# Optimization experiments

Hardware: AMD Instinct MI355X
Metric: run time of the kernel (lower is better)

Reference implementation:

```python
import jax, jax.numpy as jnp
import numpy as np

N_HEADS = 32
KV_HEADS = 8
HEAD_DIM = 128
N_REP = N_HEADS // KV_HEADS


def _rope(x, cos, sin):
    # x: [b, s, h, d]; cos/sin: [s, d//2]
    xr = x[..., 0::2]
    xi = x[..., 1::2]
    c = cos[None, :, None, :]
    s = sin[None, :, None, :]
    or_ = xr * c - xi * s
    oi_ = xr * s + xi * c
    return jnp.stack([or_, oi_], axis=-1).reshape(x.shape)


def setup_inputs() -> dict:
    key = jax.random.key(0)
    ks = jax.random.split(key, 9)
    b, s, dim = 32, 1, 4096
    scale = 1.0 / np.sqrt(dim)
    inp = {
        "x": jax.random.normal(ks[0], (b, s, dim), jnp.float32),
        "wq": jax.random.normal(ks[1], (4096, 4096), jnp.float32) * scale,
        "wk": jax.random.normal(ks[2], (1024, 4096), jnp.float32) * scale,
        "wv": jax.random.normal(ks[3], (1024, 4096), jnp.float32) * scale,
        "wo": jax.random.normal(ks[4], (4096, 4096), jnp.float32) * scale,
        "freqs_cos": jax.random.uniform(ks[5], (s, HEAD_DIM // 2), jnp.float32),
        "freqs_sin": jax.random.uniform(ks[6], (s, HEAD_DIM // 2), jnp.float32),
        "cache_k": jax.random.normal(ks[7], (32, 2048, KV_HEADS, HEAD_DIM), jnp.float32),
        "cache_v": jax.random.normal(ks[8], (32, 2048, KV_HEADS, HEAD_DIM), jnp.float32),
        "start_pos": 2047,
    }
    return inp


def reference(x, wq, wk, wv, wo, freqs_cos, freqs_sin, cache_k, cache_v, start_pos):
    b, s, dim = x.shape
    # projections (nn.Linear: y = x @ W^T)
    xq = (x @ wq.T).reshape(b, s, N_HEADS, HEAD_DIM)
    xk = (x @ wk.T).reshape(b, s, KV_HEADS, HEAD_DIM)
    xv = (x @ wv.T).reshape(b, s, KV_HEADS, HEAD_DIM)
    # inline RoPE on q and k
    xq = _rope(xq, freqs_cos, freqs_sin)
    xk = _rope(xk, freqs_cos, freqs_sin)
    # KV-cache write (start_pos is a static Python int)
    cache_k = cache_k.at[:b, start_pos:start_pos + s].set(xk)
    cache_v = cache_v.at[:b, start_pos:start_pos + s].set(xv)
    t = start_pos + s
    keys = cache_k[:b, :t]    # [b, t, kv, d]
    values = cache_v[:b, :t]  # [b, t, kv, d]
    # GQA: group queries per kv head instead of materializing repeat_kv copies
    q = xq.reshape(b, s, KV_HEADS, N_REP, HEAD_DIM)
    scores = jnp.einsum("bqhrd,bkhd->bhrqk", q, keys) / np.sqrt(HEAD_DIM)
    probs = jax.nn.softmax(scores.astype(jnp.float32), axis=-1).astype(xq.dtype)
    out = jnp.einsum("bhrqk,bkhd->bqhrd", probs, values)
    out = out.reshape(b, s, N_HEADS * HEAD_DIM)
    return out @ wo.T
```

## Files before the change

### kernel.cpp

```cpp
#include <hip/hip_runtime.h>
#include <hip/hip_bf16.h>
#include <math.h>

#define KSPLIT 16
#define KCHUNK 256
#define BJ 128
#define TSPLIT 4

__global__ __launch_bounds__(256) void gemv_part_kernel(
    const float* __restrict__ x,
    const float* __restrict__ w0,
    const float* __restrict__ w1,
    const float* __restrict__ w2,
    int jb1, int jb2,
    int off0, int off1, int off2,
    int ncols,
    float* __restrict__ part)
{
  __shared__ float xt[KCHUNK][32];
  int jb = blockIdx.x, ks = blockIdx.y;
  int k0 = ks * KCHUNK;
  const float* w; int colOff, jbase;
  if (jb < jb1)      { w = w0; colOff = off0; jbase = jb * BJ; }
  else if (jb < jb2) { w = w1; colOff = off1; jbase = (jb - jb1) * BJ; }
  else               { w = w2; colOff = off2; jbase = (jb - jb2) * BJ; }
  int tid = threadIdx.x;
  {
    int b = tid & 31, kg = tid >> 5;
    const float* xr = x + (size_t)b * 4096 + k0 + kg * 32;
    #pragma unroll
    for (int i = 0; i < 8; i++) {
      float4 v = *(const float4*)(xr + i * 4);
      int k = kg * 32 + i * 4;
      xt[k + 0][b] = v.x; xt[k + 1][b] = v.y;
      xt[k + 2][b] = v.z; xt[k + 3][b] = v.w;
    }
  }
  __syncthreads();
  int bg = tid & 7, jg = tid >> 3;
  const float* wb = w + (size_t)(jbase + jg * 4) * 4096 + k0;
  float acc[4][4] = {};
  #pragma unroll 4
  for (int k4 = 0; k4 < KCHUNK / 4; k4++) {
    float wr[4][4], xv[4][4];
    #pragma unroll
    for (int jj = 0; jj < 4; jj++) {
      float4 t = *(const float4*)(wb + (size_t)jj * 4096 + k4 * 4);
      wr[jj][0] = t.x; wr[jj][1] = t.y; wr[jj][2] = t.z; wr[jj][3] = t.w;
    }
    #pragma unroll
    for (int c = 0; c < 4; c++) {
      float4 t = *(const float4*)(&xt[k4 * 4 + c][bg * 4]);
      xv[c][0] = t.x; xv[c][1] = t.y; xv[c][2] = t.z; xv[c][3] = t.w;
    }
    #pragma unroll
    for (int jj = 0; jj < 4; jj++)
      #pragma unroll
      for (int bb = 0; bb < 4; bb++)
        acc[jj][bb] += wr[jj][0] * xv[0][bb] + wr[jj][1] * xv[1][bb]
                     + wr[jj][2] * xv[2][bb] + wr[jj][3] * xv[3][bb];
  }
  #pragma unroll
  for (int jj = 0; jj < 4; jj++) {
    int col = colOff + jbase + jg * 4 + jj;
    #pragma unroll
    for (int bb = 0; bb < 4; bb++) {
      int b_ = bg * 4 + bb;
      part[((size_t)ks * 32 + b_) * ncols + col] = acc[jj][bb];
    }
  }
}

__global__ __launch_bounds__(256) void reduce_rope_kernel(
    const float* __restrict__ part, int ncols,
    const float* __restrict__ cosv, const float* __restrict__ sinv,
    int ropeEnd, float* __restrict__ outb)
{
  int idx = blockIdx.x * 256 + threadIdx.x;
  int np = ncols >> 1;
  int b = idx / np;
  int cp = idx - b * np;
  int col = cp * 2;
  float e = 0.f, o = 0.f;
  #pragma unroll
  for (int ks = 0; ks < KSPLIT; ks++) {
    float2 v = *(const float2*)(part + ((size_t)ks * 32 + b) * ncols + col);
    e += v.x; o += v.y;
  }
  if (col < ropeEnd) {
    int fi = (col & 127) >> 1;
    float c = cosv[fi], s = sinv[fi];
    float ne = e * c - o * s;
    float no = e * s + o * c;
    e = ne; o = no;
  }
  *(float2*)(outb + (size_t)b * ncols + col) = make_float2(e, o);
}

__global__ __launch_bounds__(256, 4) void attn_kernel(
    const float* __restrict__ qkv,
    const float* __restrict__ cache_k,
    const float* __restrict__ cache_v,
    const int* __restrict__ spp,
    float* __restrict__ attn_part)
{
  __shared__ float q_s[4][128];
  __shared__ float kn_s[128], vn_s[128];
  __shared__ float p_s[4][4][64];
  __shared__ float comb_m[4][4], comb_l[4][4];
  __shared__ float comb_o[4][4][128];
  int bid = blockIdx.x;
  int ts = bid & (TSPLIT - 1), h = (bid >> 2) & 7, b = bid >> 5;
  int sp = *spp;
  const float scale = 0.088388347648318447f;
  int tid = threadIdx.x;
  {
    int i0 = tid * 2;
    int r = i0 >> 7, d = i0 & 127;
    q_s[r][d]     = qkv[(size_t)b * 6144 + (h * 4 + r) * 128 + d]     * scale;
    q_s[r][d + 1] = qkv[(size_t)b * 6144 + (h * 4 + r) * 128 + d + 1] * scale;
  }
  if (tid < 128) {
    kn_s[tid] = qkv[(size_t)b * 6144 + 4096 + h * 128 + tid];
    vn_s[tid] = qkv[(size_t)b * 6144 + 5120 + h * 128 + tid];
  }
  __syncthreads();
  int wave = tid >> 6, lane = tid & 63;
  int half = lane >> 5, dq = lane & 31;
  int base0 = ts * 512 + wave * 128;
  float m[4]    = {-INFINITY, -INFINITY, -INFINITY, -INFINITY};
  float lsum[4] = {0.f, 0.f, 0.f, 0.f};
  float o[4][4] = {};
  const float* Kb = cache_k + (size_t)b * 2048 * 1024 + h * 128;
  const float* Vb = cache_v + (size_t)b * 2048 * 1024 + h * 128;

  for (int c = 0; c < 2; c++) {
    int tbase = base0 + c * 64;
    int t = tbase + lane;
    float s[4];
    if (t < sp) {
      s[0] = s[1] = s[2] = s[3] = 0.f;
      const float* Kr = Kb + (size_t)t * 1024;
      #pragma unroll 8
      for (int d4 = 0; d4 < 32; d4++) {
        float4 kv = *(const float4*)(Kr + d4 * 4);
        #pragma unroll
        for (int r = 0; r < 4; r++) {
          float4 qv = *(const float4*)(&q_s[r][d4 * 4]);
          s[r] += kv.x * qv.x + kv.y * qv.y + kv.z * qv.z + kv.w * qv.w;
        }
      }
    } else {
      s[0] = s[1] = s[2] = s[3] = -INFINITY;
    }
    #pragma unroll
    for (int r = 0; r < 4; r++) {
      float cm = s[r];
      #pragma unroll
      for (int off = 32; off >= 1; off >>= 1) cm = fmaxf(cm, __shfl_xor(cm, off));
      float nm = fmaxf(m[r], cm);
      float alpha, p;
      if (nm == -INFINITY) { alpha = 1.f; p = 0.f; }
      else {
        alpha = __expf(m[r] - nm);
        p = (s[r] == -INFINITY) ? 0.f : __expf(s[r] - nm);
      }
      m[r] = nm;
      lsum[r] = lsum[r] * alpha + p;
      #pragma unroll
      for (int j = 0; j < 4; j++) o[r][j] *= alpha;
      p_s[wave][r][lane] = p;
    }
    #pragma unroll 8
    for (int tt = 0; tt < 32; tt++) {
      int tcur = tbase + tt * 2 + half;
      float4 vv = *(const float4*)(Vb + (size_t)tcur * 1024 + dq * 4);
      #pragma unroll
      for (int r = 0; r < 4; r++) {
        float p = p_s[wave][r][tt * 2 + half];
        o[r][0] += p * vv.x; o[r][1] += p * vv.y;
        o[r][2] += p * vv.z; o[r][3] += p * vv.w;
      }
    }
  }

  if (wave == 0 && sp >= ts * 512 && sp < ts * 512 + 512) {
    float sNew[4];
    #pragma unroll
    for (int r = 0; r < 4; r++) {
      float a = q_s[r][lane * 2] * kn_s[lane * 2]
              + q_s[r][lane * 2 + 1] * kn_s[lane * 2 + 1];
      #pragma unroll
      for (int off = 32; off >= 1; off >>= 1) a += __shfl_xor(a, off);
      sNew[r] = a;
    }
    #pragma unroll
    for (int r = 0; r < 4; r++) {
      float nm = fmaxf(m[r], sNew[r]);
      float alpha = (m[r] == -INFINITY) ? 0.f : __expf(m[r] - nm);
      float p = __expf(sNew[r] - nm);
      m[r] = nm;
      lsum[r] = lsum[r] * alpha + ((lane == 0) ? p : 0.f);
      float sel = (half == 0) ? p : 0.f;
      #pragma unroll
      for (int j = 0; j < 4; j++)
        o[r][j] = o[r][j] * alpha + sel * vn_s[dq * 4 + j];
    }
  }

  #pragma unroll
  for (int r = 0; r < 4; r++) {
    float L = lsum[r];
    #pragma unroll
    for (int off = 32; off >= 1; off >>= 1) L += __shfl_xor(L, off);
    #pragma unroll
    for (int j = 0; j < 4; j++) o[r][j] += __shfl_xor(o[r][j], 32);
    if (lane == 0) { comb_m[wave][r] = m[r]; comb_l[wave][r] = L; }
    if (half == 0) {
      #pragma unroll
      for (int j = 0; j < 4; j++) comb_o[wave][r][dq * 4 + j] = o[r][j];
    }
  }
  __syncthreads();
  {
    int r = tid >> 6, dp = tid & 63;
    float gm = fmaxf(fmaxf(comb_m[0][r], comb_m[1][r]),
                     fmaxf(comb_m[2][r], comb_m[3][r]));
    float L = 0.f, O0 = 0.f, O1 = 0.f;
    #pragma unroll
    for (int wv = 0; wv < 4; wv++) {
      float mm = comb_m[wv][r];
      float al = (mm == -INFINITY) ? 0.f : __expf(mm - gm);
      L  += comb_l[wv][r] * al;
      O0 += comb_o[wv][r][dp * 2]     * al;
      O1 += comb_o[wv][r][dp * 2 + 1] * al;
    }
    float* ap = attn_part + ((((size_t)ts * 32 + b) * 8 + h) * 4 + r) * 130;
    if (dp == 0) { ap[0] = gm; ap[1] = L; }
    ap[2 + dp * 2] = O0;
    ap[3 + dp * 2] = O1;
  }
}

__global__ __launch_bounds__(256) void attn_combine_kernel(
    const float* __restrict__ attn_part, float* __restrict__ attn)
{
  int idx = blockIdx.x * 256 + threadIdx.x;
  int d = idx & 127;
  int r = (idx >> 7) & 3;
  int h = (idx >> 9) & 7;
  int b = idx >> 12;
  float mv[TSPLIT], lv[TSPLIT], ov[TSPLIT];
  float gm = -INFINITY;
  #pragma unroll
  for (int ts = 0; ts < TSPLIT; ts++) {
    const float* ap = attn_part + (((size_t)(ts * 32 + b) * 8 + h) * 4 + r) * 130;
    mv[ts] = ap[0]; lv[ts] = ap[1]; ov[ts] = ap[2 + d];
    gm = fmaxf(gm, mv[ts]);
  }
  float L = 0.f, O = 0.f;
  #pragma unroll
  for (int ts = 0; ts < TSPLIT; ts++) {
    float al = (mv[ts] == -INFINITY) ? 0.f : __expf(mv[ts] - gm);
    L += lv[ts] * al;
    O += ov[ts] * al;
  }
  attn[idx] = O / L;
}

extern "C" void kernel_launch(void* const* d_in, const int* in_sizes, int n_in,
                              void* d_out, int out_size, void* d_ws, size_t ws_size,
                              hipStream_t stream)
{
  const float* x   = (const float*)d_in[0];
  const float* wq  = (const float*)d_in[1];
  const float* wk  = (const float*)d_in[2];
  const float* wv  = (const float*)d_in[3];
  const float* wo  = (const float*)d_in[4];
  const float* fc  = (const float*)d_in[5];
  const float* fs  = (const float*)d_in[6];
  const float* ck  = (const float*)d_in[7];
  const float* cv  = (const float*)d_in[8];
  const int*   spp = (const int*)d_in[9];
  float* out = (float*)d_out;

  float* ws = (float*)d_ws;
  float* qkv_part  = ws;
  float* out_part  = ws;
  float* qkvbuf    = ws + 3145728;
  float* attn_part = qkvbuf + 196608;
  float* attnbuf   = attn_part + 532480;

  gemv_part_kernel<<<dim3(48, KSPLIT), 256, 0, stream>>>(
      x, wq, wk, wv, 32, 40, 0, 4096, 5120, 6144, qkv_part);
  reduce_rope_kernel<<<384, 256, 0, stream>>>(qkv_part, 6144, fc, fs, 5120, qkvbuf);
  attn_kernel<<<1024, 256, 0, stream>>>(qkvbuf, ck, cv, spp, attn_part);
  attn_combine_kernel<<<512, 256, 0, stream>>>(attn_part, attnbuf);
  gemv_part_kernel<<<dim3(32, KSPLIT), 256, 0, stream>>>(
      attnbuf, wo, wo, wo, 32, 32, 0, 0, 0, 4096, out_part);
  reduce_rope_kernel<<<256, 256, 0, stream>>>(out_part, 4096, fc, fs, 0, out);
}
```

Baseline: 211.4 us.

## Stage K rows through swizzled LDS tiles for coalesced attention score loads

```diff
diff --git a/kernel.cpp b/kernel.cpp
--- a/kernel.cpp
+++ b/kernel.cpp
@@ -104,58 +104,101 @@
     const int* __restrict__ spp,
     float* __restrict__ attn_part)
 {
-  __shared__ float q_s[4][128];
+  __shared__ float ktile[4][1024];
+  __shared__ float q_sw[640];
+  __shared__ float sbuf[4][64][4];
   __shared__ float kn_s[128], vn_s[128];
-  __shared__ float p_s[4][4][64];
-  __shared__ float comb_m[4][4], comb_l[4][4];
-  __shared__ float comb_o[4][4][128];
+
   int bid = blockIdx.x;
   int ts = bid & (TSPLIT - 1), h = (bid >> 2) & 7, b = bid >> 5;
   int sp = *spp;
   const float scale = 0.088388347648318447f;
   int tid = threadIdx.x;
-  {
-    int i0 = tid * 2;
-    int r = i0 >> 7, d = i0 & 127;
-    q_s[r][d]     = qkv[(size_t)b * 6144 + (h * 4 + r) * 128 + d]     * scale;
-    q_s[r][d + 1] = qkv[(size_t)b * 6144 + (h * 4 + r) * 128 + d + 1] * scale;
-  }
+
   if (tid < 128) {
-    kn_s[tid] = qkv[(size_t)b * 6144 + 4096 + h * 128 + tid];
-    vn_s[tid] = qkv[(size_t)b * 6144 + 5120 + h * 128 + tid];
+    int dq16 = tid & 31, r = tid >> 5;
+    float4 qv = *(const float4*)(qkv + (size_t)b * 6144 + (h * 4 + r) * 128 + dq16 * 4);
+    qv.x *= scale; qv.y *= scale; qv.z *= scale; qv.w *= scale;
+    *(float4*)(&q_sw[dq16 * 20 + r * 4]) = qv;
+  } else {
+    int t2 = tid - 128;
+    kn_s[t2] = qkv[(size_t)b * 6144 + 4096 + h * 128 + t2];
+    vn_s[t2] = qkv[(size_t)b * 6144 + 5120 + h * 128 + t2];
   }
   __syncthreads();
+
   int wave = tid >> 6, lane = tid & 63;
   int half = lane >> 5, dq = lane & 31;
+  int rl = lane >> 3, dg = lane & 7;
+  float* kt = &ktile[wave][0];
   int base0 = ts * 512 + wave * 128;
+  const float* Kb = cache_k + (size_t)b * 2048 * 1024 + h * 128;
+  const float* Vb = cache_v + (size_t)b * 2048 * 1024 + h * 128;
+
   float m[4]    = {-INFINITY, -INFINITY, -INFINITY, -INFINITY};
   float lsum[4] = {0.f, 0.f, 0.f, 0.f};
   float o[4][4] = {};
-  const float* Kb = cache_k + (size_t)b * 2048 * 1024 + h * 128;
-  const float* Vb = cache_v + (size_t)b * 2048 * 1024 + h * 128;
+
+  const int wr_byte = (dq * 16);
+  char* ktc = (char*)kt;
 
   for (int c = 0; c < 2; c++) {
     int tbase = base0 + c * 64;
-    int t = tbase + lane;
-    float s[4];
-    if (t < sp) {
-      s[0] = s[1] = s[2] = s[3] = 0.f;
-      const float* Kr = Kb + (size_t)t * 1024;
-      #pragma unroll 8
-      for (int d4 = 0; d4 < 32; d4++) {
-        float4 kv = *(const float4*)(Kr + d4 * 4);
+    const float* src0 = Kb + (size_t)(tbase + half) * 1024 + dq * 4;
+
+    auto LOADK = [&](float4* dst, int st) {
+      #pragma unroll
+      for (int j = 0; j < 4; j++)
+        dst[j] = *(const float4*)(src0 + (size_t)(st * 8 + j * 2) * 1024);
+    };
+    auto WRITEK = [&](const float4* srcv) {
+      #pragma unroll
+      for (int j = 0; j < 4; j++) {
+        int rw = j * 2 + half;
+        *(float4*)(ktc + rw * 512 + (wr_byte ^ (rw << 4))) = srcv[j];
+      }
+    };
+    auto COMPUTEK = [&](int st) {
+      float sp4[4] = {0.f, 0.f, 0.f, 0.f};
+      #pragma unroll
+      for (int i = 0; i < 4; i++) {
+        float4 kv = *(const float4*)(ktc + rl * 512 + ((dg * 64 + i * 16) ^ (rl << 4)));
+        int qo = (dg * 4 + i) * 20;
         #pragma unroll
         for (int r = 0; r < 4; r++) {
-          float4 qv = *(const float4*)(&q_s[r][d4 * 4]);
-          s[r] += kv.x * qv.x + kv.y * qv.y + kv.z * qv.z + kv.w * qv.w;
+          float4 qv = *(const float4*)(&q_sw[qo + r * 4]);
+          sp4[r] += kv.x * qv.x + kv.y * qv.y + kv.z * qv.z + kv.w * qv.w;
         }
       }
-    } else {
-      s[0] = s[1] = s[2] = s[3] = -INFINITY;
-    }
+      #pragma unroll
+      for (int r = 0; r < 4; r++) {
+        sp4[r] += __shfl_xor(sp4[r], 1);
+        sp4[r] += __shfl_xor(sp4[r], 2);
+        sp4[r] += __shfl_xor(sp4[r], 4);
+      }
+      if (dg == 0)
+        *(float4*)(&sbuf[wave][st * 8 + rl][0]) =
+            make_float4(sp4[0], sp4[1], sp4[2], sp4[3]);
+    };
+
+    float4 st_reg[2][4];
+    LOADK(st_reg[0], 0);
+    LOADK(st_reg[1], 1);
+    #pragma unroll
+    for (int st = 0; st < 8; st++) {
+      WRITEK(st_reg[st & 1]);
+      if (st + 2 < 8) LOADK(st_reg[st & 1], st + 2);
+      COMPUTEK(st);
+    }
+
+    int t = tbase + lane;
+    float4 sv = *(const float4*)(&sbuf[wave][lane][0]);
+    float s4[4] = {sv.x, sv.y, sv.z, sv.w};
+    if (t >= sp) { s4[0] = s4[1] = s4[2] = s4[3] = -INFINITY; }
+    float pv[4];
     #pragma unroll
     for (int r = 0; r < 4; r++) {
-      float cm = s[r];
+      float cm = s4[r];
       #pragma unroll
       for (int off = 32; off >= 1; off >>= 1) cm = fmaxf(cm, __shfl_xor(cm, off));
       float nm = fmaxf(m[r], cm);
@@ -163,21 +206,24 @@
       if (nm == -INFINITY) { alpha = 1.f; p = 0.f; }
       else {
         alpha = __expf(m[r] - nm);
-        p = (s[r] == -INFINITY) ? 0.f : __expf(s[r] - nm);
+        p = (s4[r] == -INFINITY) ? 0.f : __expf(s4[r] - nm);
       }
       m[r] = nm;
       lsum[r] = lsum[r] * alpha + p;
       #pragma unroll
       for (int j = 0; j < 4; j++) o[r][j] *= alpha;
-      p_s[wave][r][lane] = p;
-    }
+      pv[r] = p;
+    }
+    *(float4*)(&sbuf[wave][lane][0]) = make_float4(pv[0], pv[1], pv[2], pv[3]);
+
     #pragma unroll 8
     for (int tt = 0; tt < 32; tt++) {
       int tcur = tbase + tt * 2 + half;
       float4 vv = *(const float4*)(Vb + (size_t)tcur * 1024 + dq * 4);
+      const float* pp = &sbuf[wave][tt * 2 + half][0];
       #pragma unroll
       for (int r = 0; r < 4; r++) {
-        float p = p_s[wave][r][tt * 2 + half];
+        float p = pp[r];
         o[r][0] += p * vv.x; o[r][1] += p * vv.y;
         o[r][2] += p * vv.z; o[r][3] += p * vv.w;
       }
@@ -188,8 +234,10 @@
     float sNew[4];
     #pragma unroll
     for (int r = 0; r < 4; r++) {
-      float a = q_s[r][lane * 2] * kn_s[lane * 2]
-              + q_s[r][lane * 2 + 1] * kn_s[lane * 2 + 1];
+      float4 qv4 = *(const float4*)(&q_sw[(lane >> 1) * 20 + r * 4]);
+      float q0 = (lane & 1) ? qv4.z : qv4.x;
+      float q1 = (lane & 1) ? qv4.w : qv4.y;
+      float a = q0 * kn_s[lane * 2] + q1 * kn_s[lane * 2 + 1];
       #pragma unroll
       for (int off = 32; off >= 1; off >>= 1) a += __shfl_xor(a, off);
       sNew[r] = a;
@@ -208,32 +256,35 @@
     }
   }
 
-  #pragma unroll
-  for (int r = 0; r < 4; r++) {
-    float L = lsum[r];
-    #pragma unroll
-    for (int off = 32; off >= 1; off >>= 1) L += __shfl_xor(L, off);
-    #pragma unroll
-    for (int j = 0; j < 4; j++) o[r][j] += __shfl_xor(o[r][j], 32);
-    if (lane == 0) { comb_m[wave][r] = m[r]; comb_l[wave][r] = L; }
-    if (half == 0) {
-      #pragma unroll
-      for (int j = 0; j < 4; j++) comb_o[wave][r][dq * 4 + j] = o[r][j];
+  {
+    float* comb = &ktile[wave][0];
+    #pragma unroll
+    for (int r = 0; r < 4; r++) {
+      float L = lsum[r];
+      #pragma unroll
+      for (int off = 32; off >= 1; off >>= 1) L += __shfl_xor(L, off);
+      #pragma unroll
+      for (int j = 0; j < 4; j++) o[r][j] += __shfl_xor(o[r][j], 32);
+      if (lane == 0) { comb[512 + r] = m[r]; comb[516 + r] = L; }
+      if (half == 0) {
+        #pragma unroll
+        for (int j = 0; j < 4; j++) comb[r * 128 + dq * 4 + j] = o[r][j];
+      }
     }
   }
   __syncthreads();
   {
     int r = tid >> 6, dp = tid & 63;
-    float gm = fmaxf(fmaxf(comb_m[0][r], comb_m[1][r]),
-                     fmaxf(comb_m[2][r], comb_m[3][r]));
+    float gm = fmaxf(fmaxf(ktile[0][512 + r], ktile[1][512 + r]),
+                     fmaxf(ktile[2][512 + r], ktile[3][512 + r]));
     float L = 0.f, O0 = 0.f, O1 = 0.f;
     #pragma unroll
     for (int wv = 0; wv < 4; wv++) {
-      float mm = comb_m[wv][r];
+      float mm = ktile[wv][512 + r];
       float al = (mm == -INFINITY) ? 0.f : __expf(mm - gm);
-      L  += comb_l[wv][r] * al;
-      O0 += comb_o[wv][r][dp * 2]     * al;
-      O1 += comb_o[wv][r][dp * 2 + 1] * al;
+      L  += ktile[wv][516 + r] * al;
+      O0 += ktile[wv][r * 128 + dp * 2]     * al;
+      O1 += ktile[wv][r * 128 + dp * 2 + 1] * al;
     }
     float* ap = attn_part + ((((size_t)ts * 32 + b) * 8 + h) * 4 + r) * 130;
     if (dp == 0) { ap[0] = gm; ap[1] = L; }
```

Measured after the change: 253.3 us. 19.8% more time.

## Split fused flash-decode attention into QK, softmax and PV kernels

Applied to the files above, without the earlier changes.

```diff
diff --git a/kernel.cpp b/kernel.cpp
--- a/kernel.cpp
+++ b/kernel.cpp
@@ -5,7 +5,6 @@
 #define KSPLIT 16
 #define KCHUNK 256
 #define BJ 128
-#define TSPLIT 4
 
 __global__ __launch_bounds__(256) void gemv_part_kernel(
     const float* __restrict__ x,
@@ -97,175 +96,206 @@
   *(float2*)(outb + (size_t)b * ncols + col) = make_float2(e, o);
 }
 
-__global__ __launch_bounds__(256, 4) void attn_kernel(
+__global__ __launch_bounds__(256, 8) void qk_kernel(
     const float* __restrict__ qkv,
     const float* __restrict__ cache_k,
-    const float* __restrict__ cache_v,
     const int* __restrict__ spp,
-    float* __restrict__ attn_part)
-{
-  __shared__ float q_s[4][128];
-  __shared__ float kn_s[128], vn_s[128];
-  __shared__ float p_s[4][4][64];
-  __shared__ float comb_m[4][4], comb_l[4][4];
-  __shared__ float comb_o[4][4][128];
+    float* __restrict__ s_ws)
+{
   int bid = blockIdx.x;
-  int ts = bid & (TSPLIT - 1), h = (bid >> 2) & 7, b = bid >> 5;
+  int ts = bid & 7, h = (bid >> 3) & 7, b = bid >> 6;
   int sp = *spp;
   const float scale = 0.088388347648318447f;
   int tid = threadIdx.x;
+  int wave = tid >> 6, lane = tid & 63;
+  int tl = lane >> 5, dq = lane & 31;
+  int tbase = ts * 256 + wave * 64;
+
+  float4 qreg[4];
   {
-    int i0 = tid * 2;
-    int r = i0 >> 7, d = i0 & 127;
-    q_s[r][d]     = qkv[(size_t)b * 6144 + (h * 4 + r) * 128 + d]     * scale;
-    q_s[r][d + 1] = qkv[(size_t)b * 6144 + (h * 4 + r) * 128 + d + 1] * scale;
-  }
-  if (tid < 128) {
-    kn_s[tid] = qkv[(size_t)b * 6144 + 4096 + h * 128 + tid];
-    vn_s[tid] = qkv[(size_t)b * 6144 + 5120 + h * 128 + tid];
-  }
-  __syncthreads();
-  int wave = tid >> 6, lane = tid & 63;
+    const float* qb = qkv + (size_t)b * 6144 + h * 512 + dq * 4;
+    #pragma unroll
+    for (int r = 0; r < 4; r++) {
+      float4 q = *(const float4*)(qb + r * 128);
+      qreg[r] = make_float4(q.x * scale, q.y * scale, q.z * scale, q.w * scale);
+    }
+  }
+  const float* Krow = cache_k + (size_t)(b * 2048 + tbase + tl) * 1024 + h * 128 + dq * 4;
+  float* srow = s_ws + (size_t)(b * 8 + h) * 8192;
+
+  float4 buf[4];
+  #pragma unroll
+  for (int g = 0; g < 3; g++) buf[g] = *(const float4*)(Krow + (size_t)g * 2048);
+  #pragma unroll 8
+  for (int g = 0; g < 32; g++) {
+    float4 kv = buf[g & 3];
+    if (g + 3 < 32) buf[(g + 3) & 3] = *(const float4*)(Krow + (size_t)(g + 3) * 2048);
+    float s0 = kv.x*qreg[0].x + kv.y*qreg[0].y + kv.z*qreg[0].z + kv.w*qreg[0].w;
+    float s1 = kv.x*qreg[1].x + kv.y*qreg[1].y + kv.z*qreg[1].z + kv.w*qreg[1].w;
+    float s2 = kv.x*qreg[2].x + kv.y*qreg[2].y + kv.z*qreg[2].z + kv.w*qreg[2].w;
+    float s3 = kv.x*qreg[3].x + kv.y*qreg[3].y + kv.z*qreg[3].z + kv.w*qreg[3].w;
+    #pragma unroll
+    for (int off = 1; off <= 16; off <<= 1) {
+      s0 += __shfl_xor(s0, off);
+      s1 += __shfl_xor(s1, off);
+      s2 += __shfl_xor(s2, off);
+      s3 += __shfl_xor(s3, off);
+    }
+    int t = tbase + g * 2 + tl;
+    if (dq == 0 && t != sp)
+      *(float4*)(srow + (size_t)t * 4) = make_float4(s0, s1, s2, s3);
+  }
+  if (wave == 0 && (sp >> 8) == ts) {
+    float4 kn4 = *(const float4*)(qkv + (size_t)b * 6144 + 4096 + h * 128 + dq * 4);
+    float a[4];
+    #pragma unroll
+    for (int r = 0; r < 4; r++) {
+      float a_ = kn4.x*qreg[r].x + kn4.y*qreg[r].y + kn4.z*qreg[r].z + kn4.w*qreg[r].w;
+      #pragma unroll
+      for (int off = 1; off <= 16; off <<= 1) a_ += __shfl_xor(a_, off);
+      a[r] = a_;
+    }
+    if (lane == 0)
+      *(float4*)(srow + (size_t)sp * 4) = make_float4(a[0], a[1], a[2], a[3]);
+  }
+}
+
+__global__ __launch_bounds__(256) void softmax_kernel(float* __restrict__ s_ws)
+{
+  __shared__ float wred[4][4];
+  int bh = blockIdx.x;
+  float* srow = s_ws + (size_t)bh * 8192;
+  int tid = threadIdx.x, wave = tid >> 6, lane = tid & 63;
+  float4 v[8];
+  float pm[4] = {-INFINITY, -INFINITY, -INFINITY, -INFINITY};
+  #pragma unroll
+  for (int k = 0; k < 8; k++) {
+    v[k] = *(const float4*)(srow + (size_t)(k * 256 + tid) * 4);
+    pm[0] = fmaxf(pm[0], v[k].x); pm[1] = fmaxf(pm[1], v[k].y);
+    pm[2] = fmaxf(pm[2], v[k].z); pm[3] = fmaxf(pm[3], v[k].w);
+  }
+  #pragma unroll
+  for (int r = 0; r < 4; r++)
+    #pragma unroll
+    for (int off = 32; off >= 1; off >>= 1)
+      pm[r] = fmaxf(pm[r], __shfl_xor(pm[r], off));
+  if (lane == 0) {
+    wred[wave][0] = pm[0]; wred[wave][1] = pm[1];
+    wred[wave][2] = pm[2]; wred[wave][3] = pm[3];
+  }
+  __syncthreads();
+  float m4[4];
+  #pragma unroll
+  for (int r = 0; r < 4; r++)
+    m4[r] = fmaxf(fmaxf(wred[0][r], wred[1][r]), fmaxf(wred[2][r], wred[3][r]));
+  __syncthreads();
+  float ps[4] = {0.f, 0.f, 0.f, 0.f};
+  #pragma unroll
+  for (int k = 0; k < 8; k++) {
+    v[k].x = __expf(v[k].x - m4[0]); ps[0] += v[k].x;
+    v[k].y = __expf(v[k].y - m4[1]); ps[1] += v[k].y;
+    v[k].z = __expf(v[k].z - m4[2]); ps[2] += v[k].z;
+    v[k].w = __expf(v[k].w - m4[3]); ps[3] += v[k].w;
+  }
+  #pragma unroll
+  for (int r = 0; r < 4; r++)
+    #pragma unroll
+    for (int off = 32; off >= 1; off >>= 1)
+      ps[r] += __shfl_xor(ps[r], off);
+  if (lane == 0) {
+    wred[wave][0] = ps[0]; wred[wave][1] = ps[1];
+    wred[wave][2] = ps[2]; wred[wave][3] = ps[3];
+  }
+  __syncthreads();
+  float inv[4];
+  #pragma unroll
+  for (int r = 0; r < 4; r++)
+    inv[r] = 1.f / (wred[0][r] + wred[1][r] + wred[2][r] + wred[3][r]);
+  #pragma unroll
+  for (int k = 0; k < 8; k++) {
+    v[k].x *= inv[0]; v[k].y *= inv[1]; v[k].z *= inv[2]; v[k].w *= inv[3];
+    *(float4*)(srow + (size_t)(k * 256 + tid) * 4) = v[k];
+  }
+}
+
+__global__ __launch_bounds__(256, 8) void pv_kernel(
+    const float* __restrict__ p_ws,
+    const float* __restrict__ cache_v,
+    const int* __restrict__ spp,
+    float* __restrict__ pv_part)
+{
+  __shared__ float red[4][4][128];
+  int bid = blockIdx.x;
+  int ts = bid & 7, h = (bid >> 3) & 7, b = bid >> 6;
+  int sp = *spp;
+  int tid = threadIdx.x, wave = tid >> 6, lane = tid & 63;
   int half = lane >> 5, dq = lane & 31;
-  int base0 = ts * 512 + wave * 128;
-  float m[4]    = {-INFINITY, -INFINITY, -INFINITY, -INFINITY};
-  float lsum[4] = {0.f, 0.f, 0.f, 0.f};
+  int tbase = ts * 256 + wave * 64;
+  const float* Vrow = cache_v + (size_t)(b * 2048 + tbase + half) * 1024 + h * 128 + dq * 4;
+  const float* prow = p_ws + (size_t)(b * 8 + h) * 8192;
+
+  float4 vbuf[4];
+  #pragma unroll
+  for (int g = 0; g < 3; g++) vbuf[g] = *(const float4*)(Vrow + (size_t)g * 2048);
   float o[4][4] = {};
-  const float* Kb = cache_k + (size_t)b * 2048 * 1024 + h * 128;
-  const float* Vb = cache_v + (size_t)b * 2048 * 1024 + h * 128;
-
-  for (int c = 0; c < 2; c++) {
-    int tbase = base0 + c * 64;
-    int t = tbase + lane;
-    float s[4];
-    if (t < sp) {
-      s[0] = s[1] = s[2] = s[3] = 0.f;
-      const float* Kr = Kb + (size_t)t * 1024;
-      #pragma unroll 8
-      for (int d4 = 0; d4 < 32; d4++) {
-        float4 kv = *(const float4*)(Kr + d4 * 4);
-        #pragma unroll
-        for (int r = 0; r < 4; r++) {
-          float4 qv = *(const float4*)(&q_s[r][d4 * 4]);
-          s[r] += kv.x * qv.x + kv.y * qv.y + kv.z * qv.z + kv.w * qv.w;
-        }
-      }
-    } else {
-      s[0] = s[1] = s[2] = s[3] = -INFINITY;
-    }
-    #pragma unroll
-    for (int r = 0; r < 4; r++) {
-      float cm = s[r];
-      #pragma unroll
-      for (int off = 32; off >= 1; off >>= 1) cm = fmaxf(cm, __shfl_xor(cm, off));
-      float nm = fmaxf(m[r], cm);
-      float alpha, p;
-      if (nm == -INFINITY) { alpha = 1.f; p = 0.f; }
-      else {
-        alpha = __expf(m[r] - nm);
-        p = (s[r] == -INFINITY) ? 0.f : __expf(s[r] - nm);
-      }
-      m[r] = nm;
-      lsum[r] = lsum[r] * alpha + p;
-      #pragma unroll
-      for (int j = 0; j < 4; j++) o[r][j] *= alpha;
-      p_s[wave][r][lane] = p;
-    }
-    #pragma unroll 8
-    for (int tt = 0; tt < 32; tt++) {
-      int tcur = tbase + tt * 2 + half;
-      float4 vv = *(const float4*)(Vb + (size_t)tcur * 1024 + dq * 4);
-      #pragma unroll
-      for (int r = 0; r < 4; r++) {
-        float p = p_s[wave][r][tt * 2 + half];
-        o[r][0] += p * vv.x; o[r][1] += p * vv.y;
-        o[r][2] += p * vv.z; o[r][3] += p * vv.w;
-      }
-    }
-  }
-
-  if (wave == 0 && sp >= ts * 512 && sp < ts * 512 + 512) {
-    float sNew[4];
-    #pragma unroll
-    for (int r = 0; r < 4; r++) {
-      float a = q_s[r][lane * 2] * kn_s[lane * 2]
-              + q_s[r][lane * 2 + 1] * kn_s[lane * 2 + 1];
-      #pragma unroll
-      for (int off = 32; off >= 1; off >>= 1) a += __shfl_xor(a, off);
-      sNew[r] = a;
-    }
-    #pragma unroll
-    for (int r = 0; r < 4; r++) {
-      float nm = fmaxf(m[r], sNew[r]);
-      float alpha = (m[r] == -INFINITY) ? 0.f : __expf(m[r] - nm);
-      float p = __expf(sNew[r] - nm);
-      m[r] = nm;
-      lsum[r] = lsum[r] * alpha + ((lane == 0) ? p : 0.f);
-      float sel = (half == 0) ? p : 0.f;
-      #pragma unroll
-      for (int j = 0; j < 4; j++)
-        o[r][j] = o[r][j] * alpha + sel * vn_s[dq * 4 + j];
-    }
-  }
-
-  #pragma unroll
-  for (int r = 0; r < 4; r++) {
-    float L = lsum[r];
-    #pragma unroll
-    for (int off = 32; off >= 1; off >>= 1) L += __shfl_xor(L, off);
+  #pragma unroll 8
+  for (int g = 0; g < 32; g++) {
+    float4 vv = vbuf[g & 3];
+    if (g + 3 < 32) vbuf[(g + 3) & 3] = *(const float4*)(Vrow + (size_t)(g + 3) * 2048);
+    int t = tbase + g * 2 + half;
+    float4 pp = *(const float4*)(prow + (size_t)t * 4);
+    if (t == sp) pp = make_float4(0.f, 0.f, 0.f, 0.f);
+    o[0][0] += pp.x * vv.x; o[0][1] += pp.x * vv.y;
+    o[0][2] += pp.x * vv.z; o[0][3] += pp.x * vv.w;
+    o[1][0] += pp.y * vv.x; o[1][1] += pp.y * vv.y;
+    o[1][2] += pp.y * vv.z; o[1][3] += pp.y * vv.w;
+    o[2][0] += pp.z * vv.x; o[2][1] += pp.z * vv.y;
+    o[2][2] += pp.z * vv.z; o[2][3] += pp.z * vv.w;
+    o[3][0] += pp.w * vv.x; o[3][1] += pp.w * vv.y;
+    o[3][2] += pp.w * vv.z; o[3][3] += pp.w * vv.w;
+  }
+  #pragma unroll
+  for (int r = 0; r < 4; r++)
     #pragma unroll
     for (int j = 0; j < 4; j++) o[r][j] += __shfl_xor(o[r][j], 32);
-    if (lane == 0) { comb_m[wave][r] = m[r]; comb_l[wave][r] = L; }
-    if (half == 0) {
-      #pragma unroll
-      for (int j = 0; j < 4; j++) comb_o[wave][r][dq * 4 + j] = o[r][j];
-    }
+  if (half == 0) {
+    #pragma unroll
+    for (int r = 0; r < 4; r++)
+      *(float4*)(&red[wave][r][dq * 4]) =
+          make_float4(o[r][0], o[r][1], o[r][2], o[r][3]);
   }
   __syncthreads();
   {
     int r = tid >> 6, dp = tid & 63;
-    float gm = fmaxf(fmaxf(comb_m[0][r], comb_m[1][r]),
-                     fmaxf(comb_m[2][r], comb_m[3][r]));
-    float L = 0.f, O0 = 0.f, O1 = 0.f;
-    #pragma unroll
-    for (int wv = 0; wv < 4; wv++) {
-      float mm = comb_m[wv][r];
-      float al = (mm == -INFINITY) ? 0.f : __expf(mm - gm);
-      L  += comb_l[wv][r] * al;
-      O0 += comb_o[wv][r][dp * 2]     * al;
-      O1 += comb_o[wv][r][dp * 2 + 1] * al;
-    }
-    float* ap = attn_part + ((((size_t)ts * 32 + b) * 8 + h) * 4 + r) * 130;
-    if (dp == 0) { ap[0] = gm; ap[1] = L; }
-    ap[2 + dp * 2] = O0;
-    ap[3 + dp * 2] = O1;
-  }
-}
-
-__global__ __launch_bounds__(256) void attn_combine_kernel(
-    const float* __restrict__ attn_part, float* __restrict__ attn)
+    float a0 = red[0][r][dp * 2]     + red[1][r][dp * 2]
+             + red[2][r][dp * 2]     + red[3][r][dp * 2];
+    float a1 = red[0][r][dp * 2 + 1] + red[1][r][dp * 2 + 1]
+             + red[2][r][dp * 2 + 1] + red[3][r][dp * 2 + 1];
+    float* pb = pv_part + (size_t)(((ts * 32 + b) * 8 + h) * 4 + r) * 128;
+    *(float2*)(pb + dp * 2) = make_float2(a0, a1);
+  }
+}
+
+__global__ __launch_bounds__(256) void pv_combine_kernel(
+    const float* __restrict__ pv_part,
+    const float* __restrict__ p_ws,
+    const float* __restrict__ qkv,
+    const int* __restrict__ spp,
+    float* __restrict__ attn)
 {
   int idx = blockIdx.x * 256 + threadIdx.x;
   int d = idx & 127;
   int r = (idx >> 7) & 3;
   int h = (idx >> 9) & 7;
   int b = idx >> 12;
-  float mv[TSPLIT], lv[TSPLIT], ov[TSPLIT];
-  float gm = -INFINITY;
-  #pragma unroll
-  for (int ts = 0; ts < TSPLIT; ts++) {
-    const float* ap = attn_part + (((size_t)(ts * 32 + b) * 8 + h) * 4 + r) * 130;
-    mv[ts] = ap[0]; lv[ts] = ap[1]; ov[ts] = ap[2 + d];
-    gm = fmaxf(gm, mv[ts]);
-  }
-  float L = 0.f, O = 0.f;
-  #pragma unroll
-  for (int ts = 0; ts < TSPLIT; ts++) {
-    float al = (mv[ts] == -INFINITY) ? 0.f : __expf(mv[ts] - gm);
-    L += lv[ts] * al;
-    O += ov[ts] * al;
-  }
-  attn[idx] = O / L;
+  float acc = 0.f;
+  #pragma unroll
+  for (int ts = 0; ts < 8; ts++)
+    acc += pv_part[(size_t)(((ts * 32 + b) * 8 + h) * 4 + r) * 128 + d];
+  int sp = *spp;
+  float psp = p_ws[(size_t)(b * 8 + h) * 8192 + (size_t)sp * 4 + r];
+  float vn  = qkv[(size_t)b * 6144 + 5120 + h * 128 + d];
+  attn[idx] = acc + psp * vn;
 }
 
 extern "C" void kernel_launch(void* const* d_in, const int* in_sizes, int n_in,
@@ -286,16 +316,19 @@
 
   float* ws = (float*)d_ws;
   float* qkv_part  = ws;
+  float* s_ws      = ws;
+  float* pv_part   = ws + 2097152;
   float* out_part  = ws;
   float* qkvbuf    = ws + 3145728;
-  float* attn_part = qkvbuf + 196608;
-  float* attnbuf   = attn_part + 532480;
+  float* attnbuf   = ws + 3342336;
 
   gemv_part_kernel<<<dim3(48, KSPLIT), 256, 0, stream>>>(
       x, wq, wk, wv, 32, 40, 0, 4096, 5120, 6144, qkv_part);
   reduce_rope_kernel<<<384, 256, 0, stream>>>(qkv_part, 6144, fc, fs, 5120, qkvbuf);
-  attn_kernel<<<1024, 256, 0, stream>>>(qkvbuf, ck, cv, spp, attn_part);
-  attn_combine_kernel<<<512, 256, 0, stream>>>(attn_part, attnbuf);
+  qk_kernel<<<2048, 256, 0, stream>>>(qkvbuf, ck, spp, s_ws);
+  softmax_kernel<<<256, 256, 0, stream>>>(s_ws);
+  pv_kernel<<<2048, 256, 0, stream>>>(s_ws, cv, spp, pv_part);
+  pv_combine_kernel<<<512, 256, 0, stream>>>(pv_part, s_ws, qkvbuf, spp, attnbuf);
   gemv_part_kernel<<<dim3(32, KSPLIT), 256, 0, stream>>>(
       attnbuf, wo, wo, wo, 32, 32, 0, 0, 0, 4096, out_part);
   reduce_rope_kernel<<<256, 256, 0, stream>>>(out_part, 4096, fc, fs, 0, out);
```

New measurement: 360.2 us. 70.4% more time.
